# Kernel tuning notes

Measured on AMD Instinct MI355X. Metric: run time of the kernel, lower is better.

## Reference

```python
import jax, jax.numpy as jnp
import numpy as np

N_NODES = 100000
NEG_SLOPE = 0.2


def gat_conv(x, W, att_src, att_dst, bias, src, dst, heads, out_ch):
    # x: [N, F_in]; W: [F_in, heads*out_ch]; att_*: [heads, out_ch]; bias: [heads*out_ch]
    N = x.shape[0]
    h = (x @ W).reshape(N, heads, out_ch)                 # [N, H, C]
    a_src = jnp.sum(h * att_src[None], axis=-1)           # [N, H]
    a_dst = jnp.sum(h * att_dst[None], axis=-1)           # [N, H]
    # per-edge unnormalized attention logits (PyG GATConv)
    alpha = jax.nn.leaky_relu(a_src[src] + a_dst[dst], NEG_SLOPE)   # [E, H]
    # scatter-softmax over edges grouped by destination node
    m = jax.ops.segment_max(alpha, dst, num_segments=N)   # [N, H]
    m = jnp.where(jnp.isfinite(m), m, 0.0)
    e = jnp.exp(alpha - m[dst])                           # [E, H]
    s = jax.ops.segment_sum(e, dst, num_segments=N)       # [N, H]
    alpha = e / (s[dst] + 1e-16)
    # weighted scatter-add aggregation of neighbor features
    out = jax.ops.segment_sum(alpha[:, :, None] * h[src], dst, num_segments=N)  # [N, H, C]
    return out.reshape(N, heads * out_ch) + bias


def setup_inputs() -> dict:
    key = jax.random.key(0)
    ks = jax.random.split(key, 10)
    F_in = 128
    x = jax.random.normal(ks[0], (N_NODES, F_in), dtype=jnp.float32)
    edge_index = jax.random.randint(ks[1], (2, 3200000), 0, N_NODES, dtype=jnp.int64)
    g = 0.1
    return {
        "x": x,
        "edge_index": edge_index,
        "W1": jax.random.normal(ks[2], (F_in, 32), jnp.float32) * g,
        "att_src1": jax.random.normal(ks[3], (2, 16), jnp.float32) * g,
        "att_dst1": jax.random.normal(ks[4], (2, 16), jnp.float32) * g,
        "b1": jnp.zeros((32,), jnp.float32),
        "W2": jax.random.normal(ks[5], (32, 2), jnp.float32) * g,
        "att_src2": jax.random.normal(ks[6], (1, 2), jnp.float32) * g,
        "att_dst2": jax.random.normal(ks[7], (1, 2), jnp.float32) * g,
        "b2": jnp.zeros((2,), jnp.float32),
    }


def reference(x, edge_index, W1, att_src1, att_dst1, b1, W2, att_src2, att_dst2, b2):
    N = x.shape[0]
    # add self-loops (PyG GATConv default add_self_loops=True)
    loops = jnp.arange(N, dtype=edge_index.dtype)
    src = jnp.concatenate([edge_index[0], loops])
    dst = jnp.concatenate([edge_index[1], loops])
    h = gat_conv(x, W1, att_src1, att_dst1, b1, src, dst, heads=2, out_ch=16)
    h = jax.nn.elu(h)
    h = gat_conv(h, W2, att_src2, att_dst2, b2, src, dst, heads=1, out_ch=2)
    return jax.nn.log_softmax(h, axis=1)
```

## Files before the change

kernel.cpp:

```cpp
#include <hip/hip_runtime.h>
#include <hip/hip_bf16.h>
#include <hip/hip_fp16.h>

#define LEAK   0.2f
#define NPB    200
#define CAP    8192
#define CAPSH  13
#define SBITS  17
#define SMASK  0x1FFFF
#define CHUNKB 8192

__device__ __forceinline__ unsigned pkh(float a, float b) {
    __half2 h = __floats2half2_rn(a, b);
    return *(unsigned*)&h;
}
__device__ __forceinline__ float2 uph(unsigned u) {
    __half2 h = *(__half2*)&u;
    return __half22float2(h);
}

__global__ __launch_bounds__(512) void kpre(const int* __restrict__ ei, int E, int K,
                                            int NBIN,
                                            int* __restrict__ cursor,
                                            int* __restrict__ binned,
                                            const float* __restrict__ x,
                                            const float* __restrict__ W1,
                                            const float* __restrict__ atts,
                                            const float* __restrict__ attd,
                                            uint2* __restrict__ h1h,
                                            float* __restrict__ a1s,
                                            float* __restrict__ a1d, int N) {
    __shared__ __align__(16) char smem[57380];
    int t = threadIdx.x;

    if (blockIdx.x < NBIN) {
        int* hist = (int*)smem;
        int* gb    = hist + 512;
        int* lbase = gb + 512;
        int* lcur  = lbase + 512;
        unsigned short* rbk = (unsigned short*)(lcur + 512);
        int* sv    = (int*)(rbk + CHUNKB);
        int* swt   = sv + CHUNKB;
        int* probe = swt + 8;
        hist[t] = 0;
        if (t == 0) *probe = 0;
        __syncthreads();
        if (t < 256) {
            int zc = 0;
#pragma unroll
            for (int j = 0; j < 4; j++) zc += (ei[(t * 4 + j) * 2 + 1] == 0) ? 1 : 0;
            if (zc) atomicAdd(probe, zc);
        }
        __syncthreads();
        int f = (*probe == 1024);
        int e0 = blockIdx.x * CHUNKB;
        int ss[16], dd[16];
#pragma unroll
        for (int i = 0; i < 16; i++) {
            int e = e0 + t + 512 * i;
            ss[i] = -1;
            dd[i] = 0;
            if (e < E) {
                int s, d;
                if (f) { s = ei[2 * e]; d = ei[2 * (e + E)]; }
                else   { s = ei[e];     d = ei[e + E]; }
                ss[i] = s;
                dd[i] = d;
                atomicAdd(&hist[d / NPB], 1);
            }
        }
        __syncthreads();
        int h = (t < K) ? hist[t] : 0;
        if (h) gb[t] = (t << CAPSH) + atomicAdd(&cursor[t], h);
        int xsc = h;
#pragma unroll
        for (int o = 1; o < 64; o <<= 1) {
            int y = __shfl_up(xsc, o, 64);
            if ((t & 63) >= o) xsc += y;
        }
        if ((t & 63) == 63) swt[t >> 6] = xsc;
        __syncthreads();
        int add = 0;
#pragma unroll
        for (int j = 0; j < 8; j++)
            if (j < (t >> 6)) add += swt[j];
        int lb = xsc - h + add;
        lbase[t] = lb;
        lcur[t] = lb;
        __syncthreads();
        for (int j = 0; j < h; j++) rbk[lb + j] = (unsigned short)t;
#pragma unroll
        for (int i = 0; i < 16; i++) {
            if (ss[i] >= 0) {
                int bk = dd[i] / NPB;
                int dloc = dd[i] - bk * NPB;
                int pos = atomicAdd(&lcur[bk], 1);
                sv[pos] = ss[i] | (dloc << SBITS);
            }
        }
        __syncthreads();
        int tot = min(CHUNKB, E - e0);
        for (int i = t; i < tot; i += 512) {
            int bk = rbk[i];
            int gpos = gb[bk] + (i - lbase[bk]);
            if (gpos < ((bk + 1) << CAPSH))
                binned[gpos] = sv[i];
        }
    } else {
        int b = blockIdx.x - NBIN;
        float* Ws = (float*)smem;
        float* xs = Ws + 4096;
        const float4* W4 = (const float4*)W1;
        float4* Ws4 = (float4*)Ws;
#pragma unroll
        for (int i = 0; i < 2; i++) Ws4[t + 512 * i] = W4[t + 512 * i];
        long long node0 = (long long)b * 64;
        const float4* x4 = (const float4*)x;
        float4* xs4 = (float4*)xs;
#pragma unroll
        for (int i = 0; i < 4; i++) {
            int idx = t + 512 * i;
            int row = idx >> 5, col = idx & 31;
            long long n = node0 + row;
            float4 v = make_float4(0.f, 0.f, 0.f, 0.f);
            if (n < N) v = x4[n * 32 + col];
            xs4[row * 33 + col] = v;
        }
        __syncthreads();

        int cg = t & 7, ns = t >> 3;
        const float4* xr = (const float4*)(xs + ns * 132);
        float acc[4] = {0.f, 0.f, 0.f, 0.f};
#pragma unroll 8
        for (int k4 = 0; k4 < 32; k4++) {
            float4 xa = xr[k4];
            float av[4] = {xa.x, xa.y, xa.z, xa.w};
#pragma unroll
            for (int i = 0; i < 4; i++) {
                float4 w = Ws4[(k4 * 4 + i) * 8 + cg];
                acc[0] = fmaf(av[i], w.x, acc[0]);
                acc[1] = fmaf(av[i], w.y, acc[1]);
                acc[2] = fmaf(av[i], w.z, acc[2]);
                acc[3] = fmaf(av[i], w.w, acc[3]);
            }
        }
        long long gn = node0 + ns;
        if (gn < N) h1h[gn * 8 + cg] = make_uint2(pkh(acc[0], acc[1]),
                                                  pkh(acc[2], acc[3]));
        float ps = 0.f, pd = 0.f;
#pragma unroll
        for (int i = 0; i < 4; i++) {
            ps = fmaf(acc[i], atts[cg * 4 + i], ps);
            pd = fmaf(acc[i], attd[cg * 4 + i], pd);
        }
#pragma unroll
        for (int m = 1; m < 4; m <<= 1) {
            ps += __shfl_xor(ps, m, 64);
            pd += __shfl_xor(pd, m, 64);
        }
        if ((cg & 3) == 0) {
            int hd = cg >> 2;
            if (gn < N) { a1s[gn * 2 + hd] = ps; a1d[gn * 2 + hd] = pd; }
        }
    }
}

__global__ __launch_bounds__(1024) void kfused(const int* __restrict__ cursor,
                                               const int* __restrict__ binned,
                                               const uint2* __restrict__ h1h,
                                               const float* __restrict__ a1s,
                                               const float* __restrict__ a1d,
                                               const float* __restrict__ b1,
                                               const float* __restrict__ W2,
                                               const float* __restrict__ as2,
                                               const float* __restrict__ ad2,
                                               float4* __restrict__ pk,
                                               int* __restrict__ srcs,
                                               int* __restrict__ od, int N) {
    __shared__ int lsrc[CAP];
    __shared__ int ldeg[NPB], lcur[NPB], loff[NPB];
    __shared__ int swt[4];
    int b = blockIdx.x, t = threadIdx.x;
    int node0 = b * NPB;
    int nn = min(NPB, N - node0);
    int cnt = cursor[b];
    if (cnt > CAP) cnt = CAP;
    const int* bb = binned + ((long long)b << CAPSH);
    if (t < NPB) ldeg[t] = 0;
    __syncthreads();
    int pv[8];
#pragma unroll
    for (int j = 0; j < 8; j++) {
        int i = t + 1024 * j;
        pv[j] = (i < cnt) ? bb[i] : -1;
        if (pv[j] >= 0) atomicAdd(&ldeg[pv[j] >> SBITS], 1);
    }
    __syncthreads();
    {
        int v = 0, xsc = 0;
        if (t < 256) {
            v = (t < nn) ? ldeg[t] : 0;
            xsc = v;
#pragma unroll
            for (int o = 1; o < 64; o <<= 1) {
                int y = __shfl_up(xsc, o, 64);
                if ((t & 63) >= o) xsc += y;
            }
            if ((t & 63) == 63) swt[t >> 6] = xsc;
        }
        __syncthreads();
        if (t < 256) {
            int add = 0;
#pragma unroll
            for (int j = 0; j < 4; j++)
                if (j < (t >> 6)) add += swt[j];
            xsc += add;
            if (t < nn) {
                int rel = xsc - v;
                loff[t] = rel;
                lcur[t] = rel;
                od[node0 + t] = rel | (v << 14);
            }
        }
        __syncthreads();
    }
#pragma unroll
    for (int j = 0; j < 8; j++) {
        if (pv[j] >= 0) {
            int pos = atomicAdd(&lcur[pv[j] >> SBITS], 1);
            lsrc[pos] = pv[j] & SMASK;
        }
    }
    __syncthreads();
    for (int i = t; i < cnt; i += 1024) srcs[((long long)b << CAPSH) + i] = lsrc[i];

    int wv = t >> 6, lane = t & 63;
    int e8 = lane >> 3, c4 = lane & 7, hd = c4 >> 2;
    bool wlane = (c4 & 3) == 0;
    for (int ni = wv; ni < nn; ni += 16) {
        int n = node0 + ni;
        float a1dn = a1d[2 * n + hd];
        int base = loff[ni], g = ldeg[ni];
        float4 acc = make_float4(0.f, 0.f, 0.f, 0.f);
        float wsum = 0.f;
        for (int tt = e8 - 1; tt < g; tt += 16) {
            int t2 = tt + 8;
            bool p2 = t2 < g;
            int s0 = (tt < 0) ? n : lsrc[base + tt];
            int s1 = p2 ? lsrc[base + t2] : s0;
            float as0 = a1s[2 * s0 + hd];
            float as1 = a1s[2 * s1 + hd];
            uint2 hb0 = h1h[(size_t)s0 * 8 + c4];
            uint2 hb1 = h1h[(size_t)s1 * 8 + c4];
            float al0 = as0 + a1dn;
            al0 = al0 > 0.f ? al0 : LEAK * al0;
            float w0 = __expf(al0);
            float al1 = as1 + a1dn;
            al1 = al1 > 0.f ? al1 : LEAK * al1;
            float w1 = p2 ? __expf(al1) : 0.f;
            float2 f01 = uph(hb0.x), f23 = uph(hb0.y);
            float2 g01 = uph(hb1.x), g23 = uph(hb1.y);
            acc.x = fmaf(w0, f01.x, acc.x);
            acc.y = fmaf(w0, f01.y, acc.y);
            acc.z = fmaf(w0, f23.x, acc.z);
            acc.w = fmaf(w0, f23.y, acc.w);
            acc.x = fmaf(w1, g01.x, acc.x);
            acc.y = fmaf(w1, g01.y, acc.y);
            acc.z = fmaf(w1, g23.x, acc.z);
            acc.w = fmaf(w1, g23.y, acc.w);
            if (wlane) wsum += w0 + w1;
        }
#pragma unroll
        for (int m = 8; m < 64; m <<= 1) {
            acc.x += __shfl_xor(acc.x, m, 64);
            acc.y += __shfl_xor(acc.y, m, 64);
            acc.z += __shfl_xor(acc.z, m, 64);
            acc.w += __shfl_xor(acc.w, m, 64);
            wsum += __shfl_xor(wsum, m, 64);
        }
        float wsH = __shfl(wsum, hd * 4, 64);
        float inv = 1.f / (wsH + 1e-16f);
        float4 bv = ((const float4*)b1)[c4];
        float4 t1;
        t1.x = acc.x * inv + bv.x;
        t1.y = acc.y * inv + bv.y;
        t1.z = acc.z * inv + bv.z;
        t1.w = acc.w * inv + bv.w;
        t1.x = t1.x > 0.f ? t1.x : __expf(t1.x) - 1.f;
        t1.y = t1.y > 0.f ? t1.y : __expf(t1.y) - 1.f;
        t1.z = t1.z > 0.f ? t1.z : __expf(t1.z) - 1.f;
        t1.w = t1.w > 0.f ? t1.w : __expf(t1.w) - 1.f;
        const float4* W24 = (const float4*)W2;
        float4 wA = W24[c4 * 2], wB = W24[c4 * 2 + 1];
        float p0 = t1.x * wA.x + t1.y * wA.z + t1.z * wB.x + t1.w * wB.z;
        float p1 = t1.x * wA.y + t1.y * wA.w + t1.z * wB.y + t1.w * wB.w;
#pragma unroll
        for (int m = 1; m < 8; m <<= 1) {
            p0 += __shfl_xor(p0, m, 64);
            p1 += __shfl_xor(p1, m, 64);
        }
        if (lane == 0)
            pk[n] = make_float4(p0 * as2[0] + p1 * as2[1], p0, p1,
                                p0 * ad2[0] + p1 * ad2[1]);
    }
}

__global__ __launch_bounds__(256) void kagg2(const int* __restrict__ od,
                                             const int* __restrict__ srcs,
                                             const float4* __restrict__ pk,
                                             const float* __restrict__ b2,
                                             float* __restrict__ out, int N) {
    int sub = threadIdx.x >> 5, k = threadIdx.x & 31;
    int n = blockIdx.x * 8 + sub;
    if (n >= N) return;
    float4 pn = pk[n];
    float adn = pn.w;
    int o = od[n];
    int base = ((n / NPB) << CAPSH) + (o & 16383);
    int g = o >> 14;
    float a0 = 0.f, a1v = 0.f, wsm = 0.f;
    for (int e = k - 1; e < g; e += 32) {
        float4 p = (e < 0) ? pn : pk[srcs[base + e]];
        float al = p.x + adn;
        al = al > 0.f ? al : LEAK * al;
        float w = __expf(al);
        a0 = fmaf(w, p.y, a0);
        a1v = fmaf(w, p.z, a1v);
        wsm += w;
    }
#pragma unroll
    for (int m = 1; m < 32; m <<= 1) {
        a0 += __shfl_xor(a0, m, 32);
        a1v += __shfl_xor(a1v, m, 32);
        wsm += __shfl_xor(wsm, m, 32);
    }
    if (k == 0) {
        float inv = 1.f / (wsm + 1e-16f);
        float o0 = a0 * inv + b2[0];
        float o1 = a1v * inv + b2[1];
        float mx = fmaxf(o0, o1);
        float lse = mx + __logf(__expf(o0 - mx) + __expf(o1 - mx));
        ((float2*)out)[n] = make_float2(o0 - lse, o1 - lse);
    }
}

extern "C" void kernel_launch(void* const* d_in, const int* in_sizes, int n_in,
                              void* d_out, int out_size, void* d_ws, size_t ws_size,
                              hipStream_t stream) {
    const float* x   = (const float*)d_in[0];
    const int*   ei  = (const int*)d_in[1];
    const float* W1  = (const float*)d_in[2];
    const float* as1 = (const float*)d_in[3];
    const float* ad1 = (const float*)d_in[4];
    const float* b1  = (const float*)d_in[5];
    const float* W2  = (const float*)d_in[6];
    const float* as2 = (const float*)d_in[7];
    const float* ad2 = (const float*)d_in[8];
    const float* b2  = (const float*)d_in[9];
    float* out = (float*)d_out;

    int N = out_size / 2;
    int E = in_sizes[1] / 2;
    int K = (N + NPB - 1) / NPB;

    float* wsp   = (float*)d_ws;
    float4* pk   = (float4*)wsp;
    uint2* h1h   = (uint2*)(pk + (size_t)N);
    float* a1s   = (float*)(h1h + (size_t)N * 8);
    float* a1d   = a1s + (size_t)N * 2;
    int* od      = (int*)(a1d + (size_t)N * 2);
    int* srcs    = od + N;
    int* binned  = srcs + (size_t)K * CAP;
    int* cursor  = binned + (size_t)K * CAP;

    int NBIN = (E + CHUNKB - 1) / CHUNKB;
    int NK1  = (N + 63) / 64;

    hipMemsetAsync(cursor, 0, K * sizeof(int), stream);
    kpre<<<NBIN + NK1, 512, 0, stream>>>(ei, E, K, NBIN, cursor, binned,
                                         x, W1, as1, ad1, h1h, a1s, a1d, N);
    kfused<<<K, 1024, 0, stream>>>(cursor, binned, h1h, a1s, a1d,
                                   b1, W2, as2, ad2, pk, srcs, od, N);
    kagg2<<<(N + 7) / 8, 256, 0, stream>>>(od, srcs, pk, b2, out, N);
}
```

Measured before the change: 224.5 us.

## Aggregate layer two directly from binned edges with shared-memory atomics

Layer two no longer needs the CSR-sorted source list and per-node offsets that the fused layer-one kernel wrote out. It now walks the raw destination-binned edge list per block and accumulates the softmax numerator and denominator in shared memory with float atomics. This drops the global writes of srcs and od and the per-node warp layout of the old aggregation, at the cost of shared-memory atomic contention and a nondeterministic summation order.

```diff
diff --git a/kernel.cpp b/kernel.cpp
--- a/kernel.cpp
+++ b/kernel.cpp
@@ -174,9 +174,7 @@
                                                const float* __restrict__ W2,
                                                const float* __restrict__ as2,
                                                const float* __restrict__ ad2,
-                                               float4* __restrict__ pk,
-                                               int* __restrict__ srcs,
-                                               int* __restrict__ od, int N) {
+                                               float4* __restrict__ pk, int N) {
     __shared__ int lsrc[CAP];
     __shared__ int ldeg[NPB], lcur[NPB], loff[NPB];
     __shared__ int swt[4];
@@ -219,7 +217,6 @@
                 int rel = xsc - v;
                 loff[t] = rel;
                 lcur[t] = rel;
-                od[node0 + t] = rel | (v << 14);
             }
         }
         __syncthreads();
@@ -232,7 +229,6 @@
         }
     }
     __syncthreads();
-    for (int i = t; i < cnt; i += 1024) srcs[((long long)b << CAPSH) + i] = lsrc[i];
 
     int wv = t >> 6, lane = t & 63;
     int e8 = lane >> 3, c4 = lane & 7, hd = c4 >> 2;
@@ -305,42 +301,49 @@
     }
 }
 
-__global__ __launch_bounds__(256) void kagg2(const int* __restrict__ od,
-                                             const int* __restrict__ srcs,
+__global__ __launch_bounds__(512) void kagg2(const int* __restrict__ cursor,
+                                             const int* __restrict__ binned,
                                              const float4* __restrict__ pk,
                                              const float* __restrict__ b2,
                                              float* __restrict__ out, int N) {
-    int sub = threadIdx.x >> 5, k = threadIdx.x & 31;
-    int n = blockIdx.x * 8 + sub;
-    if (n >= N) return;
-    float4 pn = pk[n];
-    float adn = pn.w;
-    int o = od[n];
-    int base = ((n / NPB) << CAPSH) + (o & 16383);
-    int g = o >> 14;
-    float a0 = 0.f, a1v = 0.f, wsm = 0.f;
-    for (int e = k - 1; e < g; e += 32) {
-        float4 p = (e < 0) ? pn : pk[srcs[base + e]];
-        float al = p.x + adn;
+    __shared__ float4 pkl[NPB];
+    __shared__ float accW[NPB], acc0[NPB], acc1[NPB];
+    int b = blockIdx.x, t = threadIdx.x;
+    int node0 = b * NPB;
+    int nn = min(NPB, N - node0);
+    int cnt = cursor[b];
+    if (cnt > CAP) cnt = CAP;
+    const int* bb = binned + ((long long)b << CAPSH);
+    if (t < NPB) {
+        accW[t] = 0.f;
+        acc0[t] = 0.f;
+        acc1[t] = 0.f;
+        if (t < nn) pkl[t] = pk[node0 + t];
+    }
+    __syncthreads();
+    for (int i = t; i < cnt; i += 512) {
+        int pv = bb[i];
+        int s = pv & SMASK, dloc = pv >> SBITS;
+        float4 p = pk[s];
+        float al = p.x + pkl[dloc].w;
         al = al > 0.f ? al : LEAK * al;
         float w = __expf(al);
-        a0 = fmaf(w, p.y, a0);
-        a1v = fmaf(w, p.z, a1v);
-        wsm += w;
-    }
-#pragma unroll
-    for (int m = 1; m < 32; m <<= 1) {
-        a0 += __shfl_xor(a0, m, 32);
-        a1v += __shfl_xor(a1v, m, 32);
-        wsm += __shfl_xor(wsm, m, 32);
-    }
-    if (k == 0) {
-        float inv = 1.f / (wsm + 1e-16f);
-        float o0 = a0 * inv + b2[0];
-        float o1 = a1v * inv + b2[1];
+        atomicAdd(&accW[dloc], w);
+        atomicAdd(&acc0[dloc], w * p.y);
+        atomicAdd(&acc1[dloc], w * p.z);
+    }
+    __syncthreads();
+    if (t < nn) {
+        float4 pn = pkl[t];
+        float al = pn.x + pn.w;
+        al = al > 0.f ? al : LEAK * al;
+        float w = __expf(al);
+        float inv = 1.f / (accW[t] + w + 1e-16f);
+        float o0 = (acc0[t] + w * pn.y) * inv + b2[0];
+        float o1 = (acc1[t] + w * pn.z) * inv + b2[1];
         float mx = fmaxf(o0, o1);
         float lse = mx + __logf(__expf(o0 - mx) + __expf(o1 - mx));
-        ((float2*)out)[n] = make_float2(o0 - lse, o1 - lse);
+        ((float2*)out)[node0 + t] = make_float2(o0 - lse, o1 - lse);
     }
 }
 
@@ -368,9 +371,7 @@
     uint2* h1h   = (uint2*)(pk + (size_t)N);
     float* a1s   = (float*)(h1h + (size_t)N * 8);
     float* a1d   = a1s + (size_t)N * 2;
-    int* od      = (int*)(a1d + (size_t)N * 2);
-    int* srcs    = od + N;
-    int* binned  = srcs + (size_t)K * CAP;
+    int* binned  = (int*)(a1d + (size_t)N * 2);
     int* cursor  = binned + (size_t)K * CAP;
 
     int NBIN = (E + CHUNKB - 1) / CHUNKB;
@@ -380,6 +381,6 @@
     kpre<<<NBIN + NK1, 512, 0, stream>>>(ei, E, K, NBIN, cursor, binned,
                                          x, W1, as1, ad1, h1h, a1s, a1d, N);
     kfused<<<K, 1024, 0, stream>>>(cursor, binned, h1h, a1s, a1d,
-                                   b1, W2, as2, ad2, pk, srcs, od, N);
-    kagg2<<<(N + 7) / 8, 256, 0, stream>>>(od, srcs, pk, b2, out, N);
-}
+                                   b1, W2, as2, ad2, pk, N);
+    kagg2<<<K, 512, 0, stream>>>(cursor, binned, pk, b2, out, N);
+}
```

After: 244.8 us. 1.09x slower.

## Use 4 threads per node in layer-2 aggregation with batched gathers; fold rbk fill into scatter

Applied to the files above, without the earlier changes.

The layer-2 aggregation kernel now assigns 4 lanes per destination node instead of 32. Each lane unrolls 8 edges per iteration, issuing all index and feature gathers before the compute so more loads are in flight and fewer lanes sit idle on low-degree nodes (average degree is about 33). The binning kernel drops a separate per-bucket loop that filled the reverse-bucket array and instead writes the bucket id at each atomically claimed position. The trade-offs are higher register use, a few redundant loads for masked-out edges, and a different floating-point summation order.

```diff
diff --git a/kernel.cpp b/kernel.cpp
--- a/kernel.cpp
+++ b/kernel.cpp
@@ -88,7 +88,6 @@
         lbase[t] = lb;
         lcur[t] = lb;
         __syncthreads();
-        for (int j = 0; j < h; j++) rbk[lb + j] = (unsigned short)t;
 #pragma unroll
         for (int i = 0; i < 16; i++) {
             if (ss[i] >= 0) {
@@ -96,6 +95,7 @@
                 int dloc = dd[i] - bk * NPB;
                 int pos = atomicAdd(&lcur[bk], 1);
                 sv[pos] = ss[i] | (dloc << SBITS);
+                rbk[pos] = (unsigned short)bk;
             }
         }
         __syncthreads();
@@ -310,8 +310,8 @@
                                              const float4* __restrict__ pk,
                                              const float* __restrict__ b2,
                                              float* __restrict__ out, int N) {
-    int sub = threadIdx.x >> 5, k = threadIdx.x & 31;
-    int n = blockIdx.x * 8 + sub;
+    int sub = threadIdx.x >> 2, k = threadIdx.x & 3;
+    int n = blockIdx.x * 64 + sub;
     if (n >= N) return;
     float4 pn = pk[n];
     float adn = pn.w;
@@ -319,20 +319,37 @@
     int base = ((n / NPB) << CAPSH) + (o & 16383);
     int g = o >> 14;
     float a0 = 0.f, a1v = 0.f, wsm = 0.f;
-    for (int e = k - 1; e < g; e += 32) {
-        float4 p = (e < 0) ? pn : pk[srcs[base + e]];
-        float al = p.x + adn;
-        al = al > 0.f ? al : LEAK * al;
-        float w = __expf(al);
-        a0 = fmaf(w, p.y, a0);
-        a1v = fmaf(w, p.z, a1v);
-        wsm += w;
-    }
-#pragma unroll
-    for (int m = 1; m < 32; m <<= 1) {
-        a0 += __shfl_xor(a0, m, 32);
-        a1v += __shfl_xor(a1v, m, 32);
-        wsm += __shfl_xor(wsm, m, 32);
+    for (int e0 = k - 1; e0 < g; e0 += 32) {
+        int ee[8];
+        bool qq[8];
+        int sS[8];
+#pragma unroll
+        for (int j = 0; j < 8; j++) {
+            ee[j] = e0 + 4 * j;
+            qq[j] = ee[j] < g;
+        }
+        sS[0] = (e0 < 0) ? n : srcs[base + e0];
+#pragma unroll
+        for (int j = 1; j < 8; j++) sS[j] = qq[j] ? srcs[base + ee[j]] : sS[0];
+        float4 pp[8];
+        pp[0] = (e0 < 0) ? pn : pk[sS[0]];
+#pragma unroll
+        for (int j = 1; j < 8; j++) pp[j] = pk[sS[j]];
+#pragma unroll
+        for (int j = 0; j < 8; j++) {
+            float al = pp[j].x + adn;
+            al = al > 0.f ? al : LEAK * al;
+            float w = (j == 0 || qq[j]) ? __expf(al) : 0.f;
+            a0  = fmaf(w, pp[j].y, a0);
+            a1v = fmaf(w, pp[j].z, a1v);
+            wsm += w;
+        }
+    }
+#pragma unroll
+    for (int m = 1; m < 4; m <<= 1) {
+        a0 += __shfl_xor(a0, m, 64);
+        a1v += __shfl_xor(a1v, m, 64);
+        wsm += __shfl_xor(wsm, m, 64);
     }
     if (k == 0) {
         float inv = 1.f / (wsm + 1e-16f);
@@ -381,5 +398,5 @@
                                          x, W1, as1, ad1, h1h, a1s, a1d, N);
     kfused<<<K, 1024, 0, stream>>>(cursor, binned, h1h, a1s, a1d,
                                    b1, W2, as2, ad2, pk, srcs, od, N);
-    kagg2<<<(N + 7) / 8, 256, 0, stream>>>(od, srcs, pk, b2, out, N);
-}
+    kagg2<<<(N + 63) / 64, 256, 0, stream>>>(od, srcs, pk, b2, out, N);
+}
```

Result: faster. 217.5 us (median of 2 runs) (-3.1%).
